# Kernel tuning notes

Measured on AMD Instinct MI355X. Metric: run time of the kernel, lower is better.

The kernel has to match this reference:

```python
import jax, jax.numpy as jnp
import numpy as np

SIGMAS = jnp.array([0.0001, 0.001, 0.01, 0.1, 1, 5, 10, 15, 20, 25, 30, 100], dtype=jnp.float32)


def setup_inputs() -> dict:
    key = jax.random.key(0)
    k1, k2 = jax.random.split(key)
    N, D = 4096, 256
    feature = jax.random.normal(k1, (N, D), dtype=jnp.float32)
    domain = jax.random.randint(k2, (N,), 0, 8, dtype=jnp.int64)
    return {"feature": feature, "domain": domain}


def reference(feature, domain):
    # Pairwise squared L2 distances via the Gram trick (avoids NxNxD intermediate).
    sq = jnp.sum(feature * feature, axis=1)            # [N]
    gram = feature @ feature.T                          # [N, N]
    d2 = jnp.maximum(sq[:, None] + sq[None, :] - 2.0 * gram, 0.0)  # [N, N]

    # Multi-sigma Gaussian kernel sum: sum_s exp(-d2/2 * s). Loop over the
    # small fixed set of 12 sigmas to avoid a 12xNxN intermediate.
    k = jnp.zeros_like(d2)
    for s in [0.0001, 0.001, 0.01, 0.1, 1.0, 5.0, 10.0, 15.0, 20.0, 25.0, 30.0, 100.0]:
        k = k + jnp.exp(-d2 * (0.5 * s))

    same = (domain[:, None] == domain[None, :]).astype(jnp.float32)  # [N, N]
    neg = 1.0 - same
    Ex = jnp.sum(same * k) / jnp.sum(same)
    Ey = jnp.sum(neg * k) / jnp.sum(neg)
    return Ex - Ey
```

## Files before the change

kernel.cpp:

```cpp
#include <hip/hip_runtime.h>


typedef __attribute__((ext_vector_type(8))) short short8;
typedef __attribute__((ext_vector_type(4))) float floatx4;

#define AS1 __attribute__((address_space(1)))
#define AS3 __attribute__((address_space(3)))

__device__ inline unsigned f2bf2(float lo, float hi) {
  union { float f; unsigned u; } a, b; a.f = lo; b.f = hi;
  unsigned ra = (a.u + 0x7fffu + ((a.u >> 16) & 1u)) >> 16;
  unsigned rb = (b.u + 0x7fffu + ((b.u >> 16) & 1u)) >> 16;
  return ra | (rb << 16);
}

__device__ inline float fast_exp2(float x) {
#if __has_builtin(__builtin_amdgcn_exp2f)
  return __builtin_amdgcn_exp2f(x);
#else
  return exp2f(x);
#endif
}

__global__ __launch_bounds__(256) void prep_kernel(
    const float* __restrict__ feat, uint4* __restrict__ fbt,
    float* __restrict__ sqpart, int N, int D) {
  const int tid = threadIdx.x;
  const int rt = blockIdx.x >> 2;
  const int kq = blockIdx.x & 3;
  const int r = tid & 63;
  const int nkc = D >> 3;
  __shared__ float sqp[256];
  float ss = 0.f;
  #pragma unroll
  for (int it = 0; it < 2; ++it) {
    const int kc = kq * 8 + it * 4 + (tid >> 6);
    const float4* src = (const float4*)(feat + (size_t)(rt * 64 + r) * D + kc * 8);
    float4 v0 = src[0], v1 = src[1];
    ss += v0.x*v0.x + v0.y*v0.y + v0.z*v0.z + v0.w*v0.w
        + v1.x*v1.x + v1.y*v1.y + v1.z*v1.z + v1.w*v1.w;
    uint4 o;
    o.x = f2bf2(v0.x, v0.y); o.y = f2bf2(v0.z, v0.w);
    o.z = f2bf2(v1.x, v1.y); o.w = f2bf2(v1.z, v1.w);
    fbt[(size_t)rt * nkc * 64 + kc * 64 + r] = o;
  }
  sqp[tid] = ss;
  __syncthreads();
  if (tid < 64)
    sqpart[(size_t)kq * N + rt * 64 + tid] =
        sqp[tid] + sqp[tid + 64] + sqp[tid + 128] + sqp[tid + 192];
}

__global__ __launch_bounds__(256) void mmd_main(
    const uint4* __restrict__ fbt, const float* __restrict__ sqpart,
    const int* __restrict__ dom, float2* __restrict__ partial, int N) {
  int b = blockIdx.x;
  int i = (int)((sqrtf(8.f * (float)b + 1.f) - 1.f) * 0.5f);
  while ((i + 1) * (i + 2) / 2 <= b) ++i;
  while (i * (i + 1) / 2 > b) --i;
  const int ti = b - i * (i + 1) / 2;
  const int tj = i;
  const int rowI = ti * 64, rowJ = tj * 64;

  __shared__ __align__(16) uint4 Bs[2048];
  __shared__ float sqI[64], sqJ[64];
  __shared__ int dmI[64], dmJ[64];
  __shared__ float red[8];

  const int tid = threadIdx.x;
  const int lane = tid & 63, w = tid >> 6;
  const int quad = lane >> 4, m16 = lane & 15;

  const uint4* At = fbt + (size_t)ti * 2048;
  const uint4* Bt = fbt + (size_t)tj * 2048;

  #pragma unroll
  for (int p = 0; p < 8; ++p) {
    const int base = w * 64 + p * 256;
#if __has_builtin(__builtin_amdgcn_global_load_lds)
    __builtin_amdgcn_global_load_lds(
        (const AS1 uint4*)(Bt + base + lane),
        (AS3 uint4*)(Bs + base), 16, 0, 0);
#else
    Bs[base + lane] = Bt[base + lane];
#endif
  }

  short8 afrag[8];
  #pragma unroll
  for (int s = 0; s < 8; ++s) {
    uint4 t = At[(s * 4 + quad) * 64 + w * 16 + m16];
    afrag[s] = *(short8*)&t;
  }

  if (tid < 64) {
    sqI[tid] = sqpart[rowI + tid] + sqpart[N + rowI + tid]
             + sqpart[2 * N + rowI + tid] + sqpart[3 * N + rowI + tid];
    dmI[tid] = dom[rowI + tid];
  } else if (tid < 128) {
    int t = tid - 64;
    sqJ[t] = sqpart[rowJ + t] + sqpart[N + rowJ + t]
           + sqpart[2 * N + rowJ + t] + sqpart[3 * N + rowJ + t];
    dmJ[t] = dom[rowJ + t];
  }
  __syncthreads();

  floatx4 acc[4];
  #pragma unroll
  for (int t = 0; t < 4; ++t) acc[t] = (floatx4){0.f, 0.f, 0.f, 0.f};

  const unsigned short* BsS = (const unsigned short*)Bs;
  #pragma unroll
  for (int s = 0; s < 8; ++s) {
    #pragma unroll
    for (int t = 0; t < 4; ++t) {
      short8 bf = *(const short8*)(BsS + ((size_t)((s * 4 + quad) * 64 + t * 16 + m16)) * 8);
      acc[t] = __builtin_amdgcn_mfma_f32_16x16x32_bf16(afrag[s], bf, acc[t], 0, 0, 0);
    }
  }

  const float C0 = -7.2134752e-05f, C1 = -7.2134752e-04f, C2 = -7.2134752e-03f,
              C3 = -7.2134752e-02f, C4 = -0.72134752f, C5 = -3.6067376f,
              C100 = -72.13475204f;

  float d2v[16];
  float dmin = 3.4e38f;
  #pragma unroll
  for (int t = 0; t < 4; ++t) {
    const int c = t * 16 + m16;
    const float sqc = sqJ[c];
    const int gj = rowJ + c;
    #pragma unroll
    for (int reg = 0; reg < 4; ++reg) {
      const int r = w * 16 + quad * 4 + reg;
      const int gi = rowI + r;
      float d2 = sqI[r] + sqc - 2.f * acc[t][reg];
      d2 = fmaxf(d2, 0.f);
      if (gi == gj) d2 = 0.f;
      d2v[t * 4 + reg] = d2;
      dmin = fminf(dmin, d2);
    }
  }

  float s_all = 0.f, s_same = 0.f;
  if (__builtin_expect(dmin < 64.f, 0)) {
    #pragma unroll
    for (int t = 0; t < 4; ++t) {
      const int dc = dmJ[t * 16 + m16];
      #pragma unroll
      for (int reg = 0; reg < 4; ++reg) {
        const float d2 = d2v[t * 4 + reg];
        float e0 = fast_exp2(d2 * C0), e1 = fast_exp2(d2 * C1);
        float e2 = fast_exp2(d2 * C2), e3 = fast_exp2(d2 * C3);
        float e4 = fast_exp2(d2 * C4), e5 = fast_exp2(d2 * C5);
        float e11 = fast_exp2(d2 * C100);
        float t10 = e5 * e5, t15 = t10 * e5, t20 = t10 * t10;
        float t25 = t15 * t10, t30 = t15 * t15;
        float kk = ((e0 + e1) + (e2 + e3)) + ((e4 + e5) + (t10 + t15))
                 + ((t20 + t25) + (t30 + e11));
        s_all += kk;
        if (dmI[w * 16 + quad * 4 + reg] == dc) s_same += kk;
      }
    }
  } else {
    #pragma unroll
    for (int t = 0; t < 4; ++t) {
      const int dc = dmJ[t * 16 + m16];
      #pragma unroll
      for (int reg = 0; reg < 4; ++reg) {
        const float d2 = d2v[t * 4 + reg];
        float e0 = fast_exp2(d2 * C0), e1 = fast_exp2(d2 * C1);
        float e2 = fast_exp2(d2 * C2), e3 = fast_exp2(d2 * C3);
        float kk = (e0 + e1) + (e2 + e3);
        s_all += kk;
        if (dmI[w * 16 + quad * 4 + reg] == dc) s_same += kk;
      }
    }
  }

  #pragma unroll
  for (int off = 32; off > 0; off >>= 1) {
    s_all  += __shfl_down(s_all, off);
    s_same += __shfl_down(s_same, off);
  }
  if (lane == 0) { red[w] = s_all; red[4 + w] = s_same; }
  __syncthreads();
  if (tid == 0) {
    const float wt = (ti == tj) ? 1.f : 2.f;
    float a = (red[0] + red[1] + red[2] + red[3]) * wt;
    float s = (red[4] + red[5] + red[6] + red[7]) * wt;
    partial[b] = make_float2(s, a);
  }
}

__global__ __launch_bounds__(256) void finalize_kernel(
    const float2* __restrict__ partial, int nblk,
    const int* __restrict__ dom, float* __restrict__ out, int N) {
  __shared__ int histL[16];
  __shared__ double redS[8];
  const int tid = threadIdx.x;
  if (tid < 16) histL[tid] = 0;
  __syncthreads();
  for (int i = tid; i < N; i += 256) atomicAdd(&histL[dom[i] & 15], 1);
  double as = 0.0, aa = 0.0;
  for (int i = tid; i < nblk; i += 256) {
    float2 p = partial[i];
    as += (double)p.x; aa += (double)p.y;
  }
  #pragma unroll
  for (int off = 32; off > 0; off >>= 1) {
    as += __shfl_down(as, off);
    aa += __shfl_down(aa, off);
  }
  const int w = tid >> 6;
  if ((tid & 63) == 0) { redS[w] = as; redS[4 + w] = aa; }
  __syncthreads();
  if (tid == 0) {
    double S = redS[0] + redS[1] + redS[2] + redS[3];
    double A = redS[4] + redS[5] + redS[6] + redS[7];
    double csame = 0.0;
    for (int i = 0; i < 16; ++i) { double h = (double)histL[i]; csame += h * h; }
    double call = (double)N * (double)N;
    out[0] = (float)(S / csame - (A - S) / (call - csame));
  }
}

extern "C" void kernel_launch(void* const* d_in, const int* in_sizes, int n_in,
                              void* d_out, int out_size, void* d_ws, size_t ws_size,
                              hipStream_t stream) {
  const float* feat = (const float*)d_in[0];
  const int* dom = (const int*)d_in[1];
  float* out = (float*)d_out;
  const int N = in_sizes[1];
  const int D = in_sizes[0] / N;
  const int T = N / 64;
  const int nblk = T * (T + 1) / 2;

  char* ws = (char*)d_ws;
  float2* partial = (float2*)ws;
  float* sqpart = (float*)(ws + 16640);
  uint4* fbt = (uint4*)(ws + 82176);

  prep_kernel<<<dim3(T * 4), dim3(256), 0, stream>>>(feat, fbt, sqpart, N, D);
  mmd_main<<<dim3(nblk), dim3(256), 0, stream>>>(fbt, sqpart, dom, partial, N);
  finalize_kernel<<<1, 256, 0, stream>>>(partial, nblk, dom, out, N);
}
```

Before: 79.08 us.

## Load B fragments directly from global instead of staging through LDS

The main kernel stops copying the B tile into shared memory and instead loads each MFMA B operand straight from global memory (L2/L1-cached), which drops 32 KB of LDS per block and the async LDS copy. Per-row and per-column squared norms and domain labels are hoisted into registers before the epilogue. The finalize kernel gets a specialised path for the known block count that issues all partial loads up front, overlapping them with the histogram atomics. Direct global loads may add latency and cache traffic, in exchange for higher occupancy.

```diff
diff --git a/kernel.cpp b/kernel.cpp
--- a/kernel.cpp
+++ b/kernel.cpp
@@ -3,9 +3,6 @@
 
 typedef __attribute__((ext_vector_type(8))) short short8;
 typedef __attribute__((ext_vector_type(4))) float floatx4;
-
-#define AS1 __attribute__((address_space(1)))
-#define AS3 __attribute__((address_space(3)))
 
 __device__ inline unsigned f2bf2(float lo, float hi) {
   union { float f; unsigned u; } a, b; a.f = lo; b.f = hi;
@@ -62,7 +59,6 @@
   const int tj = i;
   const int rowI = ti * 64, rowJ = tj * 64;
 
-  __shared__ __align__(16) uint4 Bs[2048];
   __shared__ float sqI[64], sqJ[64];
   __shared__ int dmI[64], dmJ[64];
   __shared__ float red[8];
@@ -73,18 +69,6 @@
 
   const uint4* At = fbt + (size_t)ti * 2048;
   const uint4* Bt = fbt + (size_t)tj * 2048;
-
-  #pragma unroll
-  for (int p = 0; p < 8; ++p) {
-    const int base = w * 64 + p * 256;
-#if __has_builtin(__builtin_amdgcn_global_load_lds)
-    __builtin_amdgcn_global_load_lds(
-        (const AS1 uint4*)(Bt + base + lane),
-        (AS3 uint4*)(Bs + base), 16, 0, 0);
-#else
-    Bs[base + lane] = Bt[base + lane];
-#endif
-  }
 
   short8 afrag[8];
   #pragma unroll
@@ -109,32 +93,44 @@
   #pragma unroll
   for (int t = 0; t < 4; ++t) acc[t] = (floatx4){0.f, 0.f, 0.f, 0.f};
 
-  const unsigned short* BsS = (const unsigned short*)Bs;
   #pragma unroll
   for (int s = 0; s < 8; ++s) {
-    #pragma unroll
-    for (int t = 0; t < 4; ++t) {
-      short8 bf = *(const short8*)(BsS + ((size_t)((s * 4 + quad) * 64 + t * 16 + m16)) * 8);
-      acc[t] = __builtin_amdgcn_mfma_f32_16x16x32_bf16(afrag[s], bf, acc[t], 0, 0, 0);
-    }
+    uint4 b0 = Bt[(s * 4 + quad) * 64 + 0 * 16 + m16];
+    uint4 b1 = Bt[(s * 4 + quad) * 64 + 1 * 16 + m16];
+    uint4 b2 = Bt[(s * 4 + quad) * 64 + 2 * 16 + m16];
+    uint4 b3 = Bt[(s * 4 + quad) * 64 + 3 * 16 + m16];
+    acc[0] = __builtin_amdgcn_mfma_f32_16x16x32_bf16(afrag[s], *(short8*)&b0, acc[0], 0, 0, 0);
+    acc[1] = __builtin_amdgcn_mfma_f32_16x16x32_bf16(afrag[s], *(short8*)&b1, acc[1], 0, 0, 0);
+    acc[2] = __builtin_amdgcn_mfma_f32_16x16x32_bf16(afrag[s], *(short8*)&b2, acc[2], 0, 0, 0);
+    acc[3] = __builtin_amdgcn_mfma_f32_16x16x32_bf16(afrag[s], *(short8*)&b3, acc[3], 0, 0, 0);
   }
 
   const float C0 = -7.2134752e-05f, C1 = -7.2134752e-04f, C2 = -7.2134752e-03f,
               C3 = -7.2134752e-02f, C4 = -0.72134752f, C5 = -3.6067376f,
               C100 = -72.13475204f;
 
+  float sIr[4], sJr[4];
+  int dIr[4], dJr[4];
+  #pragma unroll
+  for (int reg = 0; reg < 4; ++reg) {
+    const int r = w * 16 + quad * 4 + reg;
+    sIr[reg] = sqI[r]; dIr[reg] = dmI[r];
+  }
+  #pragma unroll
+  for (int t = 0; t < 4; ++t) {
+    const int c = t * 16 + m16;
+    sJr[t] = sqJ[c]; dJr[t] = dmJ[c];
+  }
+
   float d2v[16];
   float dmin = 3.4e38f;
   #pragma unroll
   for (int t = 0; t < 4; ++t) {
-    const int c = t * 16 + m16;
-    const float sqc = sqJ[c];
-    const int gj = rowJ + c;
+    const int gj = rowJ + t * 16 + m16;
     #pragma unroll
     for (int reg = 0; reg < 4; ++reg) {
-      const int r = w * 16 + quad * 4 + reg;
-      const int gi = rowI + r;
-      float d2 = sqI[r] + sqc - 2.f * acc[t][reg];
+      const int gi = rowI + w * 16 + quad * 4 + reg;
+      float d2 = sIr[reg] + sJr[t] - 2.f * acc[t][reg];
       d2 = fmaxf(d2, 0.f);
       if (gi == gj) d2 = 0.f;
       d2v[t * 4 + reg] = d2;
@@ -146,7 +142,6 @@
   if (__builtin_expect(dmin < 64.f, 0)) {
     #pragma unroll
     for (int t = 0; t < 4; ++t) {
-      const int dc = dmJ[t * 16 + m16];
       #pragma unroll
       for (int reg = 0; reg < 4; ++reg) {
         const float d2 = d2v[t * 4 + reg];
@@ -159,13 +154,12 @@
         float kk = ((e0 + e1) + (e2 + e3)) + ((e4 + e5) + (t10 + t15))
                  + ((t20 + t25) + (t30 + e11));
         s_all += kk;
-        if (dmI[w * 16 + quad * 4 + reg] == dc) s_same += kk;
+        if (dIr[reg] == dJr[t]) s_same += kk;
       }
     }
   } else {
     #pragma unroll
     for (int t = 0; t < 4; ++t) {
-      const int dc = dmJ[t * 16 + m16];
       #pragma unroll
       for (int reg = 0; reg < 4; ++reg) {
         const float d2 = d2v[t * 4 + reg];
@@ -173,7 +167,7 @@
         float e2 = fast_exp2(d2 * C2), e3 = fast_exp2(d2 * C3);
         float kk = (e0 + e1) + (e2 + e3);
         s_all += kk;
-        if (dmI[w * 16 + quad * 4 + reg] == dc) s_same += kk;
+        if (dIr[reg] == dJr[t]) s_same += kk;
       }
     }
   }
@@ -201,12 +195,28 @@
   const int tid = threadIdx.x;
   if (tid < 16) histL[tid] = 0;
   __syncthreads();
-  for (int i = tid; i < N; i += 256) atomicAdd(&histL[dom[i] & 15], 1);
+
   double as = 0.0, aa = 0.0;
-  for (int i = tid; i < nblk; i += 256) {
-    float2 p = partial[i];
-    as += (double)p.x; aa += (double)p.y;
-  }
+  if (nblk == 2080) {
+    float2 v[8];
+    #pragma unroll
+    for (int k = 0; k < 8; ++k) v[k] = partial[tid + (k << 8)];
+    const bool has9 = tid < (2080 - 2048);
+    float2 v8 = has9 ? partial[tid + 2048] : make_float2(0.f, 0.f);
+    #pragma unroll 4
+    for (int i = tid; i < N; i += 256) atomicAdd(&histL[dom[i] & 15], 1);
+    #pragma unroll
+    for (int k = 0; k < 8; ++k) { as += (double)v[k].x; aa += (double)v[k].y; }
+    if (has9) { as += (double)v8.x; aa += (double)v8.y; }
+  } else {
+    #pragma unroll 4
+    for (int i = tid; i < N; i += 256) atomicAdd(&histL[dom[i] & 15], 1);
+    for (int i = tid; i < nblk; i += 256) {
+      float2 p = partial[i];
+      as += (double)p.x; aa += (double)p.y;
+    }
+  }
+
   #pragma unroll
   for (int off = 32; off > 0; off >>= 1) {
     as += __shfl_down(as, off);
```

Result: no change. 78.28 us (median of 3 runs) (-1.0%).
